# Kernel optimization log

Hardware: AMD Instinct MI355X
Metric: run time of the kernel (lower is better)

## Reference

```python
import jax, jax.numpy as jnp
import numpy as np

EMB = 256
N = 262144
B = 512
SLOPE = 0.01  # torch LeakyReLU default negative slope


def leaky_relu(x):
    return jnp.where(x >= 0, x, SLOPE * x)


def setup_inputs() -> dict:
    key = jax.random.key(0)
    ks = jax.random.split(key, 10)
    s = 1.0 / np.sqrt(EMB)
    s2 = 1.0 / np.sqrt(2 * EMB)
    return {
        "xg_prev": jax.random.normal(ks[0], (B, EMB), jnp.float32),
        "x": jax.random.normal(ks[1], (N, EMB), jnp.float32),
        "batch_ind": jnp.sort(jax.random.randint(ks[2], (N,), 0, B)),
        "W_mask": jax.random.uniform(ks[3], (EMB, 1), jnp.float32, -s, s),
        "b_mask": jax.random.uniform(ks[4], (1,), jnp.float32, -s, s),
        "W_feat": jax.random.uniform(ks[5], (EMB, EMB), jnp.float32, -s, s),
        "b_feat": jax.random.uniform(ks[6], (EMB,), jnp.float32, -s, s),
        "W_t": jax.random.uniform(ks[7], (2 * EMB, EMB), jnp.float32, -s2, s2),
        "b_t": jax.random.uniform(ks[8], (EMB,), jnp.float32, -s2, s2),
    }


def reference(xg_prev, x, batch_ind, W_mask, b_mask, W_feat, b_feat, W_t, b_t):
    # GlobalAttention pooling (PyG): gate = att_mask(x), feat = att_feat(x)
    gate = (x @ W_mask + b_mask)[:, 0]                      # [N]
    feat = leaky_relu(x @ W_feat + b_feat)                  # [N, EMB]
    # segment-wise stable softmax over gate per graph
    seg_max = jax.ops.segment_max(gate, batch_ind, num_segments=B)  # [B]
    seg_max = jnp.where(jnp.isfinite(seg_max), seg_max, 0.0)
    e = jnp.exp(gate - seg_max[batch_ind])                  # [N]
    denom = jax.ops.segment_sum(e, batch_ind, num_segments=B)      # [B]
    w = e / jnp.maximum(denom[batch_ind], 1e-16)            # [N]
    xg = jax.ops.segment_sum(w[:, None] * feat, batch_ind, num_segments=B)  # [B, EMB]
    # concat -> linear -> leaky_relu -> residual
    h = jnp.concatenate([xg, xg_prev], axis=1)              # [B, 2*EMB]
    out = leaky_relu(h @ W_t + b_t) + xg_prev               # [B, EMB]
    return out
```

## Files before the change

kernel.cpp:

```cpp
#include <hip/hip_runtime.h>
#include <cstdint>
#include <cstddef>

#define NROWS 262144
#define EMB 256
#define NB 512
#define NCOPY 8
#define SLOPE 0.01f

typedef __attribute__((ext_vector_type(8))) short short8;
typedef __attribute__((ext_vector_type(4))) float f32x4;

__device__ __forceinline__ unsigned short f2bf(float f) {
    unsigned u = __float_as_uint(f);
    u += 0x7FFFu + ((u >> 16) & 1u);
    return (unsigned short)(u >> 16);
}

__device__ __forceinline__ short8 pack8(const float4& lo, const float4& hi) {
    short8 s;
    s[0] = (short)f2bf(lo.x); s[1] = (short)f2bf(lo.y);
    s[2] = (short)f2bf(lo.z); s[3] = (short)f2bf(lo.w);
    s[4] = (short)f2bf(hi.x); s[5] = (short)f2bf(hi.y);
    s[6] = (short)f2bf(hi.z); s[7] = (short)f2bf(hi.w);
    return s;
}

__device__ __forceinline__ void gld16f(float* l, const float* g) {
    __builtin_amdgcn_global_load_lds(
        (const __attribute__((address_space(1))) unsigned int*)g,
        (__attribute__((address_space(3))) unsigned int*)l, 16, 0, 0);
}
__device__ __forceinline__ void gld16u(unsigned short* l, const unsigned short* g) {
    __builtin_amdgcn_global_load_lds(
        (const __attribute__((address_space(1))) unsigned int*)g,
        (__attribute__((address_space(3))) unsigned int*)l, 16, 0, 0);
}

__global__ __launch_bounds__(256) void k_prep(const float* __restrict__ Wf,
                                              unsigned short* __restrict__ Wt2,
                                              float4* __restrict__ xgPart4,
                                              float4* __restrict__ dPart4) {
    const int b = blockIdx.x, t = threadIdx.x;
    if (b < 256) {
        float v = Wf[(size_t)b * EMB + t];
        Wt2[((size_t)(b >> 3) << 11) + (t << 3) + (b & 7)] = f2bf(v);
    } else {
        const int i = (b - 256) * 256 + t;
        if (i < NCOPY * NB * EMB / 4) xgPart4[i] = (float4){0.f, 0.f, 0.f, 0.f};
        else dPart4[i - NCOPY * NB * EMB / 4] = (float4){0.f, 0.f, 0.f, 0.f};
    }
}

#define STAGE(B, KT) do {                                                         \
    {                                                                             \
        const int row_ = t >> 3, c_ = t & 7;                                      \
        const int cs_ = c_ ^ (row_ & 7);                                          \
        gld16f(&xbuf[B][t * 4], x + ((r0 + row_) << 8) + (KT) + (cs_ << 2));      \
    }                                                                             \
    _Pragma("unroll")                                                             \
    for (int q = 0; q < 2; q++) {                                                 \
        const int i_ = q * 512 + t;                                               \
        const int slab_ = i_ >> 8, off_ = i_ & 255;                               \
        gld16u(&bbuf[B][slab_ * 2048 + off_ * 8],                                 \
               Wt2 + (((size_t)((KT) >> 3) + slab_) << 11) + off_ * 8);           \
    }                                                                             \
} while (0)

__global__ __launch_bounds__(512, 6) void k_fused(const float* __restrict__ x,
                                                  const unsigned short* __restrict__ Wt2,
                                                  const float* __restrict__ wm,
                                                  const float* __restrict__ bfeat,
                                                  const int* __restrict__ bind,
                                                  float* __restrict__ dPart,
                                                  float* __restrict__ xgPart) {
    __shared__ float          xbuf[2][64 * 32];
    __shared__ unsigned short bbuf[2][32 * 256];
    __shared__ float wm_s[256];
    __shared__ float w_s[64];
    __shared__ float pxg[2][256];
    __shared__ float pden[2];
    __shared__ int   seg_s[64];
    __shared__ int   segid_s[4];
    __shared__ int   uni_s[4];

    const int t    = threadIdx.x;
    const int lane = t & 63;
    const int w    = t >> 6;
    const int wr   = w >> 1, wc = w & 1;
    const int fr   = lane & 15;
    const int fg   = lane >> 4;
    const size_t r0 = (size_t)blockIdx.x * 64;
    const int cp   = blockIdx.x & (NCOPY - 1);

    if (t < 256) { wm_s[t] = wm[t]; pxg[0][t] = 0.f; pxg[1][t] = 0.f; }
    if (t < 64) seg_s[t] = bind[r0 + t];
    if (t < 2)  pden[t] = 0.f;

    STAGE(0, 0);

    f32x4 acc[8];
#pragma unroll
    for (int n = 0; n < 8; n++) acc[n] = (f32x4){0.f, 0.f, 0.f, 0.f};
    float gp = 0.f;

#pragma unroll
    for (int s = 0; s < 8; s++) {
        const int buf = s & 1;
        if (s < 7) STAGE(buf ^ 1, (s + 1) * 32);
        if (s == 0)     asm volatile("s_waitcnt vmcnt(3) lgkmcnt(0)" ::: "memory");
        else if (s < 7) asm volatile("s_waitcnt vmcnt(3)" ::: "memory");
        else            asm volatile("s_waitcnt vmcnt(0)" ::: "memory");
        __builtin_amdgcn_sched_barrier(0);
        __builtin_amdgcn_s_barrier();
        __builtin_amdgcn_sched_barrier(0);

        const float* xb = &xbuf[buf][0];
        const unsigned short* bb = &bbuf[buf][0];

        const float4 wa  = *reinterpret_cast<const float4*>(&wm_s[s * 32 + fg * 8]);
        const float4 wbv = *reinterpret_cast<const float4*>(&wm_s[s * 32 + fg * 8 + 4]);
        const int r  = wr * 16 + fr;
        const int sl = (fg * 2) ^ (r & 7);
        const float4 lo = *reinterpret_cast<const float4*>(&xb[r * 32 + sl * 4]);
        const float4 hi = *reinterpret_cast<const float4*>(&xb[r * 32 + (sl ^ 1) * 4]);
        gp += lo.x * wa.x + lo.y * wa.y + lo.z * wa.z + lo.w * wa.w
            + hi.x * wbv.x + hi.y * wbv.y + hi.z * wbv.z + hi.w * wbv.w;
        const short8 a = pack8(lo, hi);
#pragma unroll
        for (int n = 0; n < 8; n++) {
            const short8 b = *reinterpret_cast<const short8*>(
                &bb[fg * 2048 + ((wc * 128 + n * 16 + fr) << 3)]);
            acc[n] = __builtin_amdgcn_mfma_f32_16x16x32_bf16(a, b, acc[n], 0, 0, 0);
        }

        asm volatile("s_waitcnt lgkmcnt(0)" ::: "memory");
        __builtin_amdgcn_sched_barrier(0);
        __builtin_amdgcn_s_barrier();
        __builtin_amdgcn_sched_barrier(0);
    }

    gp += __shfl_xor(gp, 16, 64);
    gp += __shfl_xor(gp, 32, 64);
    if (wc == 0 && lane < 16) w_s[wr * 16 + lane] = expf(gp);
    if (t < 4) {
        int s0 = seg_s[t * 16], ok = 1;
#pragma unroll
        for (int i = 1; i < 16; i++) ok &= (seg_s[t * 16 + i] == s0);
        segid_s[t] = s0;
        uni_s[t]   = ok;
    }
    __syncthreads();

    const int sid0 = seg_s[0];
    const int sid1 = seg_s[63];

    if (t < 4) {
        if (uni_s[t]) {
            float s = 0.f;
#pragma unroll
            for (int i = 0; i < 16; i++) s += w_s[t * 16 + i];
            const int sid = segid_s[t];
            if (sid == sid0)      atomicAdd(&pden[0], s);
            else if (sid == sid1) atomicAdd(&pden[1], s);
            else atomicAdd(&dPart[cp * NB + sid], s);
        } else {
            for (int i = 0; i < 16; i++) {
                const int sd = seg_s[t * 16 + i];
                const float e = w_s[t * 16 + i];
                if (sd == sid0)      atomicAdd(&pden[0], e);
                else if (sd == sid1) atomicAdd(&pden[1], e);
                else atomicAdd(&dPart[cp * NB + sd], e);
            }
        }
    }

    {
        const int uni  = uni_s[wr];
        const int sid  = segid_s[wr];
        const int rowb = wr * 16;
#pragma unroll
        for (int n = 0; n < 8; n++) {
            const int col = wc * 128 + n * 16 + fr;
            const float bia = bfeat[col];
            float vr[4];
#pragma unroll
            for (int r2 = 0; r2 < 4; r2++) {
                const int row = rowb + fg * 4 + r2;
                float v = acc[n][r2] + bia;
                v = (v >= 0.f) ? v : SLOPE * v;
                vr[r2] = v * w_s[row];
            }
            if (uni) {
                float s = vr[0] + vr[1] + vr[2] + vr[3];
                s += __shfl_xor(s, 16, 64);
                s += __shfl_xor(s, 32, 64);
                if (fg == 0) {
                    if (sid == sid0)      atomicAdd(&pxg[0][col], s);
                    else if (sid == sid1) atomicAdd(&pxg[1][col], s);
                    else atomicAdd(&xgPart[((size_t)(cp * NB + sid) << 8) + col], s);
                }
            } else {
#pragma unroll
                for (int r2 = 0; r2 < 4; r2++) {
                    const int sd = seg_s[rowb + fg * 4 + r2];
                    if (sd == sid0)      atomicAdd(&pxg[0][col], vr[r2]);
                    else if (sd == sid1) atomicAdd(&pxg[1][col], vr[r2]);
                    else atomicAdd(&xgPart[((size_t)(cp * NB + sd) << 8) + col], vr[r2]);
                }
            }
        }
    }
    __syncthreads();

    if (t < 256) {
        atomicAdd(&xgPart[((size_t)(cp * NB + sid0) << 8) + t], pxg[0][t]);
    } else if (sid1 != sid0) {
        atomicAdd(&xgPart[((size_t)(cp * NB + sid1) << 8) + (t - 256)], pxg[1][t - 256]);
    }
    if (t == 0) atomicAdd(&dPart[cp * NB + sid0], pden[0]);
    if (t == 1 && sid1 != sid0) atomicAdd(&dPart[cp * NB + sid1], pden[1]);
}

__global__ __launch_bounds__(256) void k_out(const float* __restrict__ xgPart,
                                             const float* __restrict__ dPart,
                                             const float* __restrict__ xgp,
                                             const float* __restrict__ Wtr,
                                             const float* __restrict__ bt,
                                             float* __restrict__ out) {
    __shared__ float h[8][512];
    const int c  = threadIdx.x;
    const int b0 = blockIdx.x * 8;
#pragma unroll
    for (int r = 0; r < 8; r++) {
        const int b = b0 + r;
        float den = 0.f, s = 0.f;
#pragma unroll
        for (int cpy = 0; cpy < NCOPY; cpy++) {
            den += dPart[cpy * NB + b];
            s   += xgPart[((size_t)(cpy * NB + b) << 8) + c];
        }
        h[r][c]       = s / fmaxf(den, 1e-16f);
        h[r][EMB + c] = xgp[(size_t)b * EMB + c];
    }
    __syncthreads();
    float acc[8] = {0.f, 0.f, 0.f, 0.f, 0.f, 0.f, 0.f, 0.f};
    for (int k = 0; k < 2 * EMB; k++) {
        float wv = Wtr[(size_t)k * EMB + c];
#pragma unroll
        for (int r = 0; r < 8; r++) acc[r] += h[r][k] * wv;
    }
#pragma unroll
    for (int r = 0; r < 8; r++) {
        float v = acc[r] + bt[c];
        v = (v >= 0.f) ? v : SLOPE * v;
        out[(size_t)(b0 + r) * EMB + c] = v + xgp[(size_t)(b0 + r) * EMB + c];
    }
}

extern "C" void kernel_launch(void* const* d_in, const int* in_sizes, int n_in,
                              void* d_out, int out_size, void* d_ws, size_t ws_size,
                              hipStream_t stream) {
    const float* xgp  = (const float*)d_in[0];
    const float* x    = (const float*)d_in[1];
    const int*   bind = (const int*)d_in[2];
    const float* Wm   = (const float*)d_in[3];
    const float* Wf   = (const float*)d_in[5];
    const float* bf   = (const float*)d_in[6];
    const float* Wtr  = (const float*)d_in[7];
    const float* bt   = (const float*)d_in[8];
    float* out = (float*)d_out;

    char* ws = (char*)d_ws;
    unsigned short* Wt2    = (unsigned short*)ws;
    float*          dPart  = (float*)(ws + 131072);
    float*          xgPart = (float*)(ws + 131072 + 16384);

    hipLaunchKernelGGL(k_prep,  dim3(256 + 1028), dim3(256), 0, stream,
                       Wf, Wt2, (float4*)xgPart, (float4*)dPart);
    hipLaunchKernelGGL(k_fused, dim3(NROWS / 64), dim3(512), 0, stream,
                       x, Wt2, Wm, bf, bind, dPart, xgPart);
    hipLaunchKernelGGL(k_out,   dim3(NB / 8),     dim3(256), 0, stream,
                       xgPart, dPart, xgp, Wtr, bt, out);
}
```

Measured before the change: 149.5 us.

## Keep full bf16 feature weight resident in LDS and loop over row tiles

The fused kernel now loads the whole 256x256 bf16 W_feat (128 KB) into shared memory once per block. It then iterates over 8 row tiles of 64 rows each, instead of restreaming weight slabs for every 64-row tile. Blocks grow to 1024 threads (16 waves), each wave covering 64 columns, so only the x tile is double-buffered from global memory. The goal is to cut repeated weight traffic and the LDS staging work per tile. The cost is roughly 160 KB of LDS per block, which allows only one block per CU, and 512 blocks with serial tile loops that may hurt latency hiding and load balance.

```diff
diff --git a/kernel.cpp b/kernel.cpp
--- a/kernel.cpp
+++ b/kernel.cpp
@@ -6,6 +6,7 @@
 #define EMB 256
 #define NB 512
 #define NCOPY 8
+#define T_TILES 8
 #define SLOPE 0.01f
 
 typedef __attribute__((ext_vector_type(8))) short short8;
@@ -52,30 +53,23 @@
     }
 }
 
-#define STAGE(B, KT) do {                                                         \
-    {                                                                             \
+#define STAGE_A(B, KT) do {                                                       \
+    if (t < 512) {                                                                \
         const int row_ = t >> 3, c_ = t & 7;                                      \
         const int cs_ = c_ ^ (row_ & 7);                                          \
         gld16f(&xbuf[B][t * 4], x + ((r0 + row_) << 8) + (KT) + (cs_ << 2));      \
     }                                                                             \
-    _Pragma("unroll")                                                             \
-    for (int q = 0; q < 2; q++) {                                                 \
-        const int i_ = q * 512 + t;                                               \
-        const int slab_ = i_ >> 8, off_ = i_ & 255;                               \
-        gld16u(&bbuf[B][slab_ * 2048 + off_ * 8],                                 \
-               Wt2 + (((size_t)((KT) >> 3) + slab_) << 11) + off_ * 8);           \
-    }                                                                             \
 } while (0)
 
-__global__ __launch_bounds__(512, 6) void k_fused(const float* __restrict__ x,
-                                                  const unsigned short* __restrict__ Wt2,
-                                                  const float* __restrict__ wm,
-                                                  const float* __restrict__ bfeat,
-                                                  const int* __restrict__ bind,
-                                                  float* __restrict__ dPart,
-                                                  float* __restrict__ xgPart) {
+__global__ __launch_bounds__(1024, 4) void k_fused(const float* __restrict__ x,
+                                                   const unsigned short* __restrict__ Wt2,
+                                                   const float* __restrict__ wm,
+                                                   const float* __restrict__ bfeat,
+                                                   const int* __restrict__ bind,
+                                                   float* __restrict__ dPart,
+                                                   float* __restrict__ xgPart) {
+    __shared__ unsigned short bbuf[32 * 2048];
     __shared__ float          xbuf[2][64 * 32];
-    __shared__ unsigned short bbuf[2][32 * 256];
     __shared__ float wm_s[256];
     __shared__ float w_s[64];
     __shared__ float pxg[2][256];
@@ -87,139 +81,157 @@
     const int t    = threadIdx.x;
     const int lane = t & 63;
     const int w    = t >> 6;
-    const int wr   = w >> 1, wc = w & 1;
+    const int wr   = w & 3;
+    const int wcg  = w >> 2;
     const int fr   = lane & 15;
     const int fg   = lane >> 4;
-    const size_t r0 = (size_t)blockIdx.x * 64;
     const int cp   = blockIdx.x & (NCOPY - 1);
 
-    if (t < 256) { wm_s[t] = wm[t]; pxg[0][t] = 0.f; pxg[1][t] = 0.f; }
-    if (t < 64) seg_s[t] = bind[r0 + t];
-    if (t < 2)  pden[t] = 0.f;
-
-    STAGE(0, 0);
-
-    f32x4 acc[8];
-#pragma unroll
-    for (int n = 0; n < 8; n++) acc[n] = (f32x4){0.f, 0.f, 0.f, 0.f};
-    float gp = 0.f;
-
-#pragma unroll
-    for (int s = 0; s < 8; s++) {
-        const int buf = s & 1;
-        if (s < 7) STAGE(buf ^ 1, (s + 1) * 32);
-        if (s == 0)     asm volatile("s_waitcnt vmcnt(3) lgkmcnt(0)" ::: "memory");
-        else if (s < 7) asm volatile("s_waitcnt vmcnt(3)" ::: "memory");
-        else            asm volatile("s_waitcnt vmcnt(0)" ::: "memory");
-        __builtin_amdgcn_sched_barrier(0);
-        __builtin_amdgcn_s_barrier();
-        __builtin_amdgcn_sched_barrier(0);
-
-        const float* xb = &xbuf[buf][0];
-        const unsigned short* bb = &bbuf[buf][0];
-
-        const float4 wa  = *reinterpret_cast<const float4*>(&wm_s[s * 32 + fg * 8]);
-        const float4 wbv = *reinterpret_cast<const float4*>(&wm_s[s * 32 + fg * 8 + 4]);
-        const int r  = wr * 16 + fr;
-        const int sl = (fg * 2) ^ (r & 7);
-        const float4 lo = *reinterpret_cast<const float4*>(&xb[r * 32 + sl * 4]);
-        const float4 hi = *reinterpret_cast<const float4*>(&xb[r * 32 + (sl ^ 1) * 4]);
-        gp += lo.x * wa.x + lo.y * wa.y + lo.z * wa.z + lo.w * wa.w
-            + hi.x * wbv.x + hi.y * wbv.y + hi.z * wbv.z + hi.w * wbv.w;
-        const short8 a = pack8(lo, hi);
-#pragma unroll
-        for (int n = 0; n < 8; n++) {
-            const short8 b = *reinterpret_cast<const short8*>(
-                &bb[fg * 2048 + ((wc * 128 + n * 16 + fr) << 3)]);
-            acc[n] = __builtin_amdgcn_mfma_f32_16x16x32_bf16(a, b, acc[n], 0, 0, 0);
-        }
-
-        asm volatile("s_waitcnt lgkmcnt(0)" ::: "memory");
-        __builtin_amdgcn_sched_barrier(0);
-        __builtin_amdgcn_s_barrier();
-        __builtin_amdgcn_sched_barrier(0);
-    }
-
-    gp += __shfl_xor(gp, 16, 64);
-    gp += __shfl_xor(gp, 32, 64);
-    if (wc == 0 && lane < 16) w_s[wr * 16 + lane] = expf(gp);
-    if (t < 4) {
-        int s0 = seg_s[t * 16], ok = 1;
-#pragma unroll
-        for (int i = 1; i < 16; i++) ok &= (seg_s[t * 16 + i] == s0);
-        segid_s[t] = s0;
-        uni_s[t]   = ok;
-    }
-    __syncthreads();
-
-    const int sid0 = seg_s[0];
-    const int sid1 = seg_s[63];
-
-    if (t < 4) {
-        if (uni_s[t]) {
-            float s = 0.f;
-#pragma unroll
-            for (int i = 0; i < 16; i++) s += w_s[t * 16 + i];
-            const int sid = segid_s[t];
-            if (sid == sid0)      atomicAdd(&pden[0], s);
-            else if (sid == sid1) atomicAdd(&pden[1], s);
-            else atomicAdd(&dPart[cp * NB + sid], s);
-        } else {
-            for (int i = 0; i < 16; i++) {
-                const int sd = seg_s[t * 16 + i];
-                const float e = w_s[t * 16 + i];
-                if (sd == sid0)      atomicAdd(&pden[0], e);
-                else if (sd == sid1) atomicAdd(&pden[1], e);
-                else atomicAdd(&dPart[cp * NB + sd], e);
-            }
-        }
-    }
-
-    {
-        const int uni  = uni_s[wr];
-        const int sid  = segid_s[wr];
-        const int rowb = wr * 16;
-#pragma unroll
-        for (int n = 0; n < 8; n++) {
-            const int col = wc * 128 + n * 16 + fr;
-            const float bia = bfeat[col];
-            float vr[4];
-#pragma unroll
-            for (int r2 = 0; r2 < 4; r2++) {
-                const int row = rowb + fg * 4 + r2;
-                float v = acc[n][r2] + bia;
-                v = (v >= 0.f) ? v : SLOPE * v;
-                vr[r2] = v * w_s[row];
-            }
-            if (uni) {
-                float s = vr[0] + vr[1] + vr[2] + vr[3];
-                s += __shfl_xor(s, 16, 64);
-                s += __shfl_xor(s, 32, 64);
-                if (fg == 0) {
-                    if (sid == sid0)      atomicAdd(&pxg[0][col], s);
-                    else if (sid == sid1) atomicAdd(&pxg[1][col], s);
-                    else atomicAdd(&xgPart[((size_t)(cp * NB + sid) << 8) + col], s);
+#pragma unroll
+    for (int q = 0; q < 8; q++) {
+        const int i = q * 1024 + t;
+        const int slab = i >> 8, off = i & 255;
+        gld16u(&bbuf[slab * 2048 + off * 8], Wt2 + ((size_t)slab << 11) + off * 8);
+    }
+    if (t < 256) wm_s[t] = wm[t];
+
+    for (int tt = 0; tt < T_TILES; tt++) {
+        const size_t r0 = ((size_t)blockIdx.x * T_TILES + tt) * 64;
+        if (tt > 0) __syncthreads();
+        if (t < 64) seg_s[t] = bind[r0 + t];
+        if (t < 256) { pxg[0][t] = 0.f; pxg[1][t] = 0.f; }
+        if (t < 2)   pden[t] = 0.f;
+
+        STAGE_A(0, 0);
+
+        f32x4 acc[4];
+#pragma unroll
+        for (int n = 0; n < 4; n++) acc[n] = (f32x4){0.f, 0.f, 0.f, 0.f};
+        float gp = 0.f;
+
+#pragma unroll
+        for (int s = 0; s < 8; s++) {
+            const int buf = s & 1;
+            if (s < 7) STAGE_A(buf ^ 1, (s + 1) * 32);
+            if (s == 0) {
+                if (tt == 0) asm volatile("s_waitcnt vmcnt(0) lgkmcnt(0)" ::: "memory");
+                else         asm volatile("s_waitcnt vmcnt(1) lgkmcnt(0)" ::: "memory");
+            } else if (s < 7) {
+                asm volatile("s_waitcnt vmcnt(1)" ::: "memory");
+            } else {
+                asm volatile("s_waitcnt vmcnt(0)" ::: "memory");
+            }
+            __builtin_amdgcn_sched_barrier(0);
+            __builtin_amdgcn_s_barrier();
+            __builtin_amdgcn_sched_barrier(0);
+
+            const float* xb = &xbuf[buf][0];
+            const float4 wa  = *reinterpret_cast<const float4*>(&wm_s[s * 32 + fg * 8]);
+            const float4 wbv = *reinterpret_cast<const float4*>(&wm_s[s * 32 + fg * 8 + 4]);
+            const int r  = wr * 16 + fr;
+            const int sl = (fg * 2) ^ (r & 7);
+            const float4 lo = *reinterpret_cast<const float4*>(&xb[r * 32 + sl * 4]);
+            const float4 hi = *reinterpret_cast<const float4*>(&xb[r * 32 + (sl ^ 1) * 4]);
+            gp += lo.x * wa.x + lo.y * wa.y + lo.z * wa.z + lo.w * wa.w
+                + hi.x * wbv.x + hi.y * wbv.y + hi.z * wbv.z + hi.w * wbv.w;
+            const short8 a = pack8(lo, hi);
+#pragma unroll
+            for (int n = 0; n < 4; n++) {
+                const short8 b = *reinterpret_cast<const short8*>(
+                    &bbuf[(s * 4 + fg) * 2048 + ((wcg * 64 + n * 16 + fr) << 3)]);
+                acc[n] = __builtin_amdgcn_mfma_f32_16x16x32_bf16(a, b, acc[n], 0, 0, 0);
+            }
+
+            asm volatile("s_waitcnt lgkmcnt(0)" ::: "memory");
+            __builtin_amdgcn_sched_barrier(0);
+            __builtin_amdgcn_s_barrier();
+            __builtin_amdgcn_sched_barrier(0);
+        }
+
+        gp += __shfl_xor(gp, 16, 64);
+        gp += __shfl_xor(gp, 32, 64);
+        if (wcg == 0 && lane < 16) w_s[wr * 16 + lane] = expf(gp);
+        if (t < 4) {
+            int s0 = seg_s[t * 16], ok = 1;
+#pragma unroll
+            for (int i = 1; i < 16; i++) ok &= (seg_s[t * 16 + i] == s0);
+            segid_s[t] = s0;
+            uni_s[t]   = ok;
+        }
+        __syncthreads();
+
+        const int sid0 = seg_s[0];
+        const int sid1 = seg_s[63];
+
+        if (t < 4) {
+            if (uni_s[t]) {
+                float s = 0.f;
+#pragma unroll
+                for (int i = 0; i < 16; i++) s += w_s[t * 16 + i];
+                const int sid = segid_s[t];
+                if (sid == sid0)      atomicAdd(&pden[0], s);
+                else if (sid == sid1) atomicAdd(&pden[1], s);
+                else atomicAdd(&dPart[cp * NB + sid], s);
+            } else {
+                for (int i = 0; i < 16; i++) {
+                    const int sd = seg_s[t * 16 + i];
+                    const float e = w_s[t * 16 + i];
+                    if (sd == sid0)      atomicAdd(&pden[0], e);
+                    else if (sd == sid1) atomicAdd(&pden[1], e);
+                    else atomicAdd(&dPart[cp * NB + sd], e);
                 }
-            } else {
+            }
+        }
+
+        {
+            const int uni  = uni_s[wr];
+            const int sid  = segid_s[wr];
+            const int rowb = wr * 16;
+#pragma unroll
+            for (int n = 0; n < 4; n++) {
+                const int col = wcg * 64 + n * 16 + fr;
+                const float bia = bfeat[col];
+                float vr[4];
 #pragma unroll
                 for (int r2 = 0; r2 < 4; r2++) {
-                    const int sd = seg_s[rowb + fg * 4 + r2];
-                    if (sd == sid0)      atomicAdd(&pxg[0][col], vr[r2]);
-                    else if (sd == sid1) atomicAdd(&pxg[1][col], vr[r2]);
-                    else atomicAdd(&xgPart[((size_t)(cp * NB + sd) << 8) + col], vr[r2]);
+                    const int row = rowb + fg * 4 + r2;
+                    float v = acc[n][r2] + bia;
+                    v = (v >= 0.f) ? v : SLOPE * v;
+                    vr[r2] = v * w_s[row];
                 }
-            }
-        }
-    }
-    __syncthreads();
-
-    if (t < 256) {
-        atomicAdd(&xgPart[((size_t)(cp * NB + sid0) << 8) + t], pxg[0][t]);
-    } else if (sid1 != sid0) {
-        atomicAdd(&xgPart[((size_t)(cp * NB + sid1) << 8) + (t - 256)], pxg[1][t - 256]);
-    }
-    if (t == 0) atomicAdd(&dPart[cp * NB + sid0], pden[0]);
-    if (t == 1 && sid1 != sid0) atomicAdd(&dPart[cp * NB + sid1], pden[1]);
+                if (uni) {
+                    float s = vr[0] + vr[1] + vr[2] + vr[3];
+                    s += __shfl_xor(s, 16, 64);
+                    s += __shfl_xor(s, 32, 64);
+                    if (fg == 0) {
+                        if (sid == sid0)      atomicAdd(&pxg[0][col], s);
+                        else if (sid == sid1) atomicAdd(&pxg[1][col], s);
+                        else atomicAdd(&xgPart[((size_t)(cp * NB + sid) << 8) + col], s);
+                    }
+                } else {
+#pragma unroll
+                    for (int r2 = 0; r2 < 4; r2++) {
+                        const int sd = seg_s[rowb + fg * 4 + r2];
+                        if (sd == sid0)      atomicAdd(&pxg[0][col], vr[r2]);
+                        else if (sd == sid1) atomicAdd(&pxg[1][col], vr[r2]);
+                        else atomicAdd(&xgPart[((size_t)(cp * NB + sd) << 8) + col], vr[r2]);
+                    }
+                }
+            }
+        }
+        __syncthreads();
+
+        if (t < 256) {
+            atomicAdd(&xgPart[((size_t)(cp * NB + sid0) << 8) + t], pxg[0][t]);
+        } else if (t < 512) {
+            if (sid1 != sid0)
+                atomicAdd(&xgPart[((size_t)(cp * NB + sid1) << 8) + (t - 256)], pxg[1][t - 256]);
+        } else if (t == 512) {
+            atomicAdd(&dPart[cp * NB + sid0], pden[0]);
+        } else if (t == 513) {
+            if (sid1 != sid0) atomicAdd(&dPart[cp * NB + sid1], pden[1]);
+        }
+    }
 }
 
 __global__ __launch_bounds__(256) void k_out(const float* __restrict__ xgPart,
@@ -276,10 +288,10 @@
     float*          dPart  = (float*)(ws + 131072);
     float*          xgPart = (float*)(ws + 131072 + 16384);
 
-    hipLaunchKernelGGL(k_prep,  dim3(256 + 1028), dim3(256), 0, stream,
+    hipLaunchKernelGGL(k_prep,  dim3(256 + 1028),              dim3(256),  0, stream,
                        Wf, Wt2, (float4*)xgPart, (float4*)dPart);
-    hipLaunchKernelGGL(k_fused, dim3(NROWS / 64), dim3(512), 0, stream,
+    hipLaunchKernelGGL(k_fused, dim3(NROWS / (64 * T_TILES)),  dim3(1024), 0, stream,
                        x, Wt2, Wm, bf, bind, dPart, xgPart);
-    hipLaunchKernelGGL(k_out,   dim3(NB / 8),     dim3(256), 0, stream,
+    hipLaunchKernelGGL(k_out,   dim3(NB / 8),                  dim3(256),  0, stream,
                        xgPart, dPart, xgp, Wtr, bt, out);
 }
```

Measured after the change: 398.6 us. 2.67x slower.
